# Kernel tuning notes

Measured on AMD Instinct MI355X. Metric: run time of the kernel, lower is better.

The kernel has to match this reference:

```python
import jax, jax.numpy as jnp
import numpy as np

B, T, D, H = 4, 2048, 1024, 16
HD = D // H  # head_dim = 64


def setup_inputs() -> dict:
    key = jax.random.key(0)
    k1, k2, k3, k4, k5 = jax.random.split(key, 5)
    scale = 1.0 / np.sqrt(D)
    return {
        "x": jax.random.normal(k1, (B, T, D), dtype=jnp.float32),
        "mask": jnp.ones((B, T), dtype=jnp.int32),
        "W_qkv": jax.random.normal(k2, (D, 3 * D), dtype=jnp.float32) * scale,
        "b_qkv": jax.random.normal(k3, (3 * D,), dtype=jnp.float32) * 0.01,
        "W_out": jax.random.normal(k4, (D, D), dtype=jnp.float32) * scale,
        "b_out": jax.random.normal(k5, (D,), dtype=jnp.float32) * 0.01,
    }


def reference(x, mask, W_qkv, b_qkv, W_out, b_out):
    Bx, Tx, Dm = x.shape
    qkv = x @ W_qkv + b_qkv                      # [B,T,3D]
    qkv = qkv.reshape(Bx, Tx, 3, H, HD)
    qkv = jnp.transpose(qkv, (2, 0, 3, 1, 4))    # [3,B,H,T,hd]
    q, k, v = qkv[0], qkv[1], qkv[2]
    att = jnp.einsum("bhqd,bhkd->bhqk", q, k) / jnp.sqrt(jnp.float32(HD))
    m = (mask[:, None, None, :] == 0)            # [B,1,1,T]
    att = jnp.where(m, jnp.float32(-1e9), att)
    att = jax.nn.softmax(att, axis=-1)
    out = jnp.einsum("bhqk,bhkd->bhqd", att, v)  # [B,H,T,hd]
    out = jnp.transpose(out, (0, 2, 1, 3)).reshape(Bx, Tx, Dm)
    return out @ W_out + b_out
```

## Files before the change

kernel.cpp:

```cpp
#include <hip/hip_runtime.h>
#include <hip/hip_bf16.h>
#include <stdint.h>

#define B_  4
#define T_  2048
#define D_  1024
#define H_  16
#define HD_ 64

typedef short s16x8 __attribute__((ext_vector_type(8)));
typedef short s16x4 __attribute__((ext_vector_type(4)));
typedef float f32x4 __attribute__((ext_vector_type(4)));

#define MFMA32(a, b, c) __builtin_amdgcn_mfma_f32_16x16x32_bf16(a, b, c, 0, 0, 0)

#if __has_builtin(__builtin_amdgcn_exp2f)
#define FEXP2(x) __builtin_amdgcn_exp2f(x)
#else
#define FEXP2(x) exp2f(x)
#endif

__device__ __forceinline__ unsigned short f2bf(float f) {
    union { float f; unsigned int u; } v; v.f = f;
    unsigned int r = v.u + 0x7fffu + ((v.u >> 16) & 1u);
    return (unsigned short)(r >> 16);
}

__device__ __forceinline__ unsigned int pkbf(float a, float b) {
    __hip_bfloat162 h = __float22bfloat162_rn(float2{a, b});
    union { __hip_bfloat162 h; unsigned int u; } v; v.h = h;
    return v.u;
}

__device__ __forceinline__ void async16(const void* g, void* l) {
    __builtin_amdgcn_global_load_lds(
        (const __attribute__((address_space(1))) unsigned int*)g,
        (__attribute__((address_space(3))) unsigned int*)l, 16, 0, 0);
}

__global__ __launch_bounds__(256)
void prep_kernel(const float* __restrict__ x, unsigned short* __restrict__ xb,
                 const float* __restrict__ Wq, unsigned short* __restrict__ Wqt,
                 const float* __restrict__ Wo, unsigned short* __restrict__ Wot) {
    const int blk = blockIdx.x;
    const int tid = threadIdx.x;
    if (blk < 8192) {
        const int i = blk * 256 + tid;
        float4 v = ((const float4*)x)[i];
        ushort4 o;
        o.x = f2bf(v.x); o.y = f2bf(v.y); o.z = f2bf(v.z); o.w = f2bf(v.w);
        ((ushort4*)xb)[i] = o;
        return;
    }
    __shared__ float t[32][33];
    const float* W; unsigned short* Wt; int K, N, bx, by;
    if (blk < 11264) {
        const int idx = blk - 8192;
        W = Wq; Wt = Wqt; K = 1024; N = 3072;
        bx = (idx % 96) * 32; by = (idx / 96) * 32;
    } else {
        const int idx = blk - 11264;
        W = Wo; Wt = Wot; K = 1024; N = 1024;
        bx = (idx % 32) * 32; by = (idx / 32) * 32;
    }
    const int tx = tid & 31, ty = tid >> 5;
    #pragma unroll
    for (int j = 0; j < 32; j += 8)
        t[ty + j][tx] = W[(size_t)(by + ty + j) * N + bx + tx];
    __syncthreads();
    #pragma unroll
    for (int j = 0; j < 32; j += 8)
        Wt[(size_t)(bx + ty + j) * K + by + tx] = f2bf(t[tx][ty + j]);
}

template <int MODE>
__global__ __launch_bounds__(256)
void gemm_bt_kernel(const unsigned short* __restrict__ A,
                    const unsigned short* __restrict__ Bt,
                    const float* __restrict__ bias,
                    float* __restrict__ Cf,
                    unsigned short* __restrict__ Qo,
                    unsigned short* __restrict__ Ko,
                    unsigned short* __restrict__ Vo,
                    int M, int N, int K) {
    __shared__ __align__(16) unsigned short SMEM[4 * 128 * 64];
    const int tid = threadIdx.x;
    const int w = tid >> 6, lane = tid & 63;
    const int laneN = lane & 15, quad = lane >> 4;
    const int rm0 = blockIdx.x * 128;
    const int rn0 = blockIdx.y * 128;
    const int wr = (w >> 1) * 64, wc = (w & 1) * 64;

    f32x4 acc[4][4] = {};

    auto issueG = [&](int kk, int bufsel) {
        unsigned short* As = SMEM + bufsel * 8192;
        unsigned short* Bs = SMEM + 16384 + bufsel * 8192;
        #pragma unroll
        for (int i = 0; i < 4; ++i) {
            const int c = i * 256 + tid;
            const int row = c >> 3, s = c & 7, g = s ^ (row & 7);
            async16(A + (size_t)(rm0 + row) * K + kk + g * 8,
                    (char*)As + (size_t)c * 16);
        }
        #pragma unroll
        for (int i = 0; i < 4; ++i) {
            const int c = i * 256 + tid;
            const int row = c >> 3, s = c & 7, g = s ^ (row & 7);
            async16(Bt + (size_t)(rn0 + row) * K + kk + g * 8,
                    (char*)Bs + (size_t)c * 16);
        }
    };

    issueG(0, 0);
    const int KI = K >> 6;
    for (int it = 0; it < KI; ++it) {
        const int buf = it & 1;
        __syncthreads();
        const unsigned short* As = SMEM + buf * 8192;
        const unsigned short* Bs = SMEM + 16384 + buf * 8192;
        s16x8 av[2][4], bv[2][4];
        #pragma unroll
        for (int h = 0; h < 2; ++h) {
            #pragma unroll
            for (int ms = 0; ms < 4; ++ms) {
                const int row = wr + ms * 16 + laneN;
                av[h][ms] = *(const s16x8*)&As[row * 64 + ((h * 4 + quad) ^ (row & 7)) * 8];
            }
            #pragma unroll
            for (int ns = 0; ns < 4; ++ns) {
                const int row = wc + ns * 16 + laneN;
                bv[h][ns] = *(const s16x8*)&Bs[row * 64 + ((h * 4 + quad) ^ (row & 7)) * 8];
            }
        }
        if (it + 1 < KI) issueG((it + 1) << 6, buf ^ 1);
        #pragma unroll
        for (int ms = 0; ms < 4; ++ms)
            #pragma unroll
            for (int ns = 0; ns < 4; ++ns) {
                acc[ms][ns] = MFMA32(av[0][ms], bv[0][ns], acc[ms][ns]);
                acc[ms][ns] = MFMA32(av[1][ms], bv[1][ns], acc[ms][ns]);
            }
    }

    if (MODE == 0) {
        #pragma unroll
        for (int ms = 0; ms < 4; ++ms) {
            const int gm0 = rm0 + wr + ms * 16 + quad * 4;
            #pragma unroll
            for (int ns = 0; ns < 4; ++ns) {
                const int gn = rn0 + wc + ns * 16 + laneN;
                const float bb = bias[gn];
                #pragma unroll
                for (int r = 0; r < 4; ++r)
                    Cf[(size_t)(gm0 + r) * N + gn] = acc[ms][ns][r] + bb;
            }
        }
    }
}

__global__ __launch_bounds__(512, 2)
void gemm256x128_qkv_kernel(const unsigned short* __restrict__ A,
                            const unsigned short* __restrict__ Bt,
                            const float* __restrict__ bias,
                            unsigned short* __restrict__ Qo,
                            unsigned short* __restrict__ Ko,
                            unsigned short* __restrict__ Vo,
                            int M, int N, int K) {
    __shared__ __align__(16) unsigned short SMEM[3 * 24576];
    const int tid = threadIdx.x;
    const int w = tid >> 6, lane = tid & 63;
    const int laneN = lane & 15, quad = lane >> 4;
    const int wm = w >> 1, wn = w & 1;
    const int rm0 = blockIdx.x * 256;
    const int rn0 = blockIdx.y * 128;

    f32x4 acc[4][4] = {};

    auto issueTile = [&](int t, int bufsel) {
        const int kk = t << 6;
        unsigned short* As = SMEM + bufsel * 24576;
        unsigned short* Bs = As + 16384;
        #pragma unroll
        for (int i = 0; i < 4; ++i) {
            const int c = i * 512 + tid;
            const int row = c >> 3, s = c & 7, g = s ^ (row & 7);
            async16(A + (size_t)(rm0 + row) * K + kk + g * 8,
                    (char*)As + (size_t)c * 16);
        }
        #pragma unroll
        for (int i = 0; i < 2; ++i) {
            const int c = i * 512 + tid;
            const int row = c >> 3, s = c & 7, g = s ^ (row & 7);
            async16(Bt + (size_t)(rn0 + row) * K + kk + g * 8,
                    (char*)Bs + (size_t)c * 16);
        }
    };

    issueTile(0, 0);
    issueTile(1, 1);
    issueTile(2, 2);
    asm volatile("s_waitcnt vmcnt(12)" ::: "memory");
    __builtin_amdgcn_s_barrier();
    asm volatile("" ::: "memory");

    const int KI = K >> 6;
    int buf = 0;
    for (int kt = 0; kt < KI; ++kt) {
        const unsigned short* As = SMEM + buf * 24576;
        const unsigned short* Bs = As + 16384;
        #pragma unroll
        for (int kh = 0; kh < 2; ++kh) {
            s16x8 av[4], bv[4];
            #pragma unroll
            for (int ns = 0; ns < 4; ++ns) {
                const int row = wn * 64 + ns * 16 + laneN;
                bv[ns] = *(const s16x8*)&Bs[row * 64 + ((kh * 4 + quad) ^ (row & 7)) * 8];
            }
            #pragma unroll
            for (int ms = 0; ms < 4; ++ms) {
                const int row = wm * 64 + ms * 16 + laneN;
                av[ms] = *(const s16x8*)&As[row * 64 + ((kh * 4 + quad) ^ (row & 7)) * 8];
            }
            __builtin_amdgcn_s_setprio(1);
            #pragma unroll
            for (int ms = 0; ms < 4; ++ms)
                #pragma unroll
                for (int ns = 0; ns < 4; ++ns)
                    acc[ms][ns] = MFMA32(av[ms], bv[ns], acc[ms][ns]);
            __builtin_amdgcn_s_setprio(0);
        }
        if (kt + 1 < KI) {
            __builtin_amdgcn_s_barrier();
            asm volatile("" ::: "memory");
            if (kt + 3 < KI) {
                issueTile(kt + 3, buf);
                asm volatile("s_waitcnt vmcnt(12)" ::: "memory");
            } else if (kt + 2 < KI) {
                asm volatile("s_waitcnt vmcnt(6)" ::: "memory");
            } else {
                asm volatile("s_waitcnt vmcnt(0)" ::: "memory");
            }
            __builtin_amdgcn_s_barrier();
            asm volatile("" ::: "memory");
        }
        buf = (buf == 2) ? 0 : buf + 1;
    }

    const int s = rn0 >> 10;
    const int bidx = rm0 >> 11, t0 = rm0 & (T_ - 1);
    if (s < 2) {
        const float fs = (s == 0) ? 0.125f * 1.44269504088896f : 1.0f;
        unsigned short* P = (s == 0) ? Qo : Ko;
        #pragma unroll
        for (int ms = 0; ms < 4; ++ms) {
            const int lm0 = wm * 64 + ms * 16 + quad * 4;
            #pragma unroll
            for (int ns = 0; ns < 4; ++ns) {
                const int gn = rn0 + wn * 64 + ns * 16 + laneN;
                const float bb = bias[gn];
                const int rr = gn & 1023, hh = rr >> 6, dd = rr & 63;
                const size_t base = ((size_t)(bidx * H_ + hh) * T_ + t0);
                #pragma unroll
                for (int r = 0; r < 4; ++r)
                    P[(base + lm0 + r) * HD_ + dd] =
                        f2bf((acc[ms][ns][r] + bb) * fs);
            }
        }
    } else {
        __syncthreads();
        #pragma unroll
        for (int ms = 0; ms < 4; ++ms) {
            const int lm0 = wm * 64 + ms * 16 + quad * 4;
            #pragma unroll
            for (int ns = 0; ns < 4; ++ns) {
                const int nl = wn * 64 + ns * 16 + laneN;
                const float bb = bias[rn0 + nl];
                const int sw = (nl & 7) << 3;
                #pragma unroll
                for (int r = 0; r < 4; ++r)
                    SMEM[nl * 256 + ((lm0 + r) ^ sw)] =
                        f2bf(acc[ms][ns][r] + bb);
            }
        }
        __syncthreads();
        const int nl = tid >> 2, part = tid & 3;
        const int hh = nl >> 6, d = nl & 63;
        const int hAbs = bidx * H_ + ((rn0 & 1023) >> 6) + hh;
        unsigned short* rowp = Vo + ((size_t)hAbs * HD_ + d) * T_ + t0;
        const int swz = nl & 7;
        #pragma unroll
        for (int j = 0; j < 8; ++j) {
            const int mgl = part * 8 + j;
            const int pg = (mgl & 24) | ((mgl & 7) ^ swz);
            const s16x8 vv = *(const s16x8*)&SMEM[nl * 256 + pg * 8];
            *(s16x8*)(rowp + mgl * 8) = vv;
        }
    }
}

__global__ __launch_bounds__(512, 4)
void attn_kernel(const unsigned short* __restrict__ Q,
                 const unsigned short* __restrict__ Kb,
                 const unsigned short* __restrict__ VT,
                 const int* __restrict__ mask,
                 unsigned short* __restrict__ Out) {
    __shared__ __align__(16) unsigned short Ks[2][64 * 64];
    __shared__ __align__(16) unsigned short Vs[2][64 * 64];
    __shared__ float biasF[T_];
    const int tid = threadIdx.x;
    const int lane = tid & 63;
    const int w = tid >> 6;
    const int laneN = lane & 15, quad = lane >> 4;
    const int x7 = laneN & 7;
    const int bh = blockIdx.x;
    const int b = bh >> 4, h = bh & 15;
    const int qbase = blockIdx.y * 256 + w * 32;

    for (int i = tid; i < T_; i += 512)
        biasF[i] = mask[b * T_ + i] ? 0.f : -1.0e9f;

    s16x8 qf[2][2];
    #pragma unroll
    for (int qg = 0; qg < 2; ++qg) {
        const size_t qoff = ((size_t)bh * T_ + qbase + qg * 16 + laneN) * HD_ + quad * 8;
        qf[qg][0] = *(const s16x8*)&Q[qoff];
        qf[qg][1] = *(const s16x8*)&Q[qoff + 32];
    }

    s16x8 ones;
    #pragma unroll
    for (int j = 0; j < 8; ++j) ones[j] = (short)0x3F80;

    const size_t kRow0 = (size_t)bh * T_ * HD_;
    const size_t vRow0 = (size_t)bh * HD_ * T_;

    auto issueTile = [&](int kt, int bufsel) {
        const int kbase = kt * 64;
        {
            const int c = tid;
            const int row = c >> 3, s = c & 7;
            const int fk = (row & 3) | (((row >> 3) & 1) << 2);
            const int g = s ^ fk;
            async16(Kb + kRow0 + (size_t)(kbase + row) * HD_ + g * 8,
                    &Ks[bufsel][c * 8]);
        }
        {
            const int c = tid;
            const int d = c >> 3, s = c & 7, g = s ^ (d & 7);
            async16(VT + vRow0 + (size_t)d * T_ + kbase + g * 8,
                    &Vs[bufsel][c * 8]);
        }
    };

    issueTile(0, 0);

    f32x4 O[2][4] = {};
    f32x4 liacc[2] = {};

    const int rowA = ((laneN >> 2) << 3) + (laneN & 3);

    #pragma unroll 2
    for (int kt = 0; kt < T_ / 64; ++kt) {
        const int buf = kt & 1;
        const int kbase = kt * 64;
        __syncthreads();
        if (kt + 1 < T_ / 64) issueTile(kt + 1, buf ^ 1);

        s16x8 pf[2][2];
        #pragma unroll
        for (int g32 = 0; g32 < 2; ++g32) {
            const int ra = g32 * 32 + rowA;
            const s16x8 kA0 = *(const s16x8*)&Ks[buf][(ra * 8 + (quad ^ x7)) * 8];
            const s16x8 kA1 = *(const s16x8*)&Ks[buf][(ra * 8 + ((4 + quad) ^ x7)) * 8];
            const s16x8 kB0 = *(const s16x8*)&Ks[buf][((ra + 4) * 8 + (quad ^ x7)) * 8];
            const s16x8 kB1 = *(const s16x8*)&Ks[buf][((ra + 4) * 8 + ((4 + quad) ^ x7)) * 8];
            const f32x4 bA = *(const f32x4*)&biasF[kbase + g32 * 32 + quad * 8];
            const f32x4 bB = *(const f32x4*)&biasF[kbase + g32 * 32 + quad * 8 + 4];
            #pragma unroll
            for (int qg = 0; qg < 2; ++qg) {
                f32x4 Sa = bA, Sb = bB;
                Sa = MFMA32(kA0, qf[qg][0], Sa);
                Sa = MFMA32(kA1, qf[qg][1], Sa);
                Sb = MFMA32(kB0, qf[qg][0], Sb);
                Sb = MFMA32(kB1, qf[qg][1], Sb);
                #pragma unroll
                for (int r = 0; r < 4; ++r) {
                    Sa[r] = FEXP2(Sa[r]);
                    Sb[r] = FEXP2(Sb[r]);
                }
                union { s16x8 v; unsigned int u[4]; } pu;
                pu.u[0] = pkbf(Sa[0], Sa[1]);
                pu.u[1] = pkbf(Sa[2], Sa[3]);
                pu.u[2] = pkbf(Sb[0], Sb[1]);
                pu.u[3] = pkbf(Sb[2], Sb[3]);
                pf[qg][g32] = pu.v;
            }
        }

        #pragma unroll
        for (int g32 = 0; g32 < 2; ++g32) {
            s16x8 vf[4];
            #pragma unroll
            for (int nt = 0; nt < 4; ++nt) {
                const int d = nt * 16 + laneN;
                vf[nt] = *(const s16x8*)&Vs[buf][(d * 8 + ((g32 * 4 + quad) ^ x7)) * 8];
            }
            #pragma unroll
            for (int qg = 0; qg < 2; ++qg) {
                #pragma unroll
                for (int nt = 0; nt < 4; ++nt)
                    O[qg][nt] = MFMA32(pf[qg][g32], vf[nt], O[qg][nt]);
                liacc[qg] = MFMA32(pf[qg][g32], ones, liacc[qg]);
            }
        }
    }

    #pragma unroll
    for (int qg = 0; qg < 2; ++qg) {
        #pragma unroll
        for (int r = 0; r < 4; ++r) {
            const float inv = 1.0f / liacc[qg][r];
            const int tq = qbase + qg * 16 + quad * 4 + r;
            #pragma unroll
            for (int nt = 0; nt < 4; ++nt)
                Out[(size_t)(b * T_ + tq) * D_ + h * HD_ + nt * 16 + laneN] =
                    f2bf(O[qg][nt][r] * inv);
        }
    }
}

extern "C" void kernel_launch(void* const* d_in, const int* in_sizes, int n_in,
                              void* d_out, int out_size, void* d_ws, size_t ws_size,
                              hipStream_t stream) {
    const float* x     = (const float*)d_in[0];
    const int*   mask  = (const int*)d_in[1];
    const float* W_qkv = (const float*)d_in[2];
    const float* b_qkv = (const float*)d_in[3];
    const float* W_out = (const float*)d_in[4];
    const float* b_out = (const float*)d_in[5];
    float* out = (float*)d_out;

    unsigned short* ws = (unsigned short*)d_ws;
    const size_t NX = (size_t)B_ * T_ * D_;
    unsigned short* xb  = ws;
    unsigned short* Qb  = xb + NX;
    unsigned short* Kb  = Qb + NX;
    unsigned short* Vtb = Kb + NX;
    unsigned short* Wqt = Vtb + NX;
    unsigned short* Wot = Wqt + (size_t)3 * D_ * D_;
    unsigned short* attn = xb;

    prep_kernel<<<12288, 256, 0, stream>>>(x, xb, W_qkv, Wqt, W_out, Wot);
    gemm256x128_qkv_kernel<<<dim3(B_ * T_ / 256, 3 * D_ / 128), 512, 0, stream>>>(
        xb, Wqt, b_qkv, Qb, Kb, Vtb, B_ * T_, 3 * D_, D_);
    attn_kernel<<<dim3(B_ * H_, T_ / 256), 512, 0, stream>>>(Qb, Kb, Vtb, mask, attn);
    gemm_bt_kernel<0><<<dim3(B_ * T_ / 128, D_ / 128), 256, 0, stream>>>(
        attn, Wot, b_out, out, nullptr, nullptr, nullptr, B_ * T_, D_, D_);
}
```

Before: 266.2 us.

## Restructure QKV GEMM pipeline with per-half barriers and issue-after-compute prefetch

Reworks the triple-buffered QKV GEMM main loop. The wait and barrier now come at the top of each iteration, and the next tile is issued after both k-halves finish computing. Barriers are added around each MFMA cluster so all waves run their MFMA phases in lockstep, a ping-pong style schedule meant to overlap LDS reads and matrix math across waves. This adds more barriers per iteration and delays when the prefetch is issued.

Result: no change. 263.8 us (-0.9%).

```diff
diff --git a/kernel.cpp b/kernel.cpp
--- a/kernel.cpp
+++ b/kernel.cpp
@@ -160,13 +160,13 @@
 }
 
 __global__ __launch_bounds__(512, 2)
-void gemm256x128_qkv_kernel(const unsigned short* __restrict__ A,
-                            const unsigned short* __restrict__ Bt,
-                            const float* __restrict__ bias,
-                            unsigned short* __restrict__ Qo,
-                            unsigned short* __restrict__ Ko,
-                            unsigned short* __restrict__ Vo,
-                            int M, int N, int K) {
+void gemm_fp_qkv_kernel(const unsigned short* __restrict__ A,
+                        const unsigned short* __restrict__ Bt,
+                        const float* __restrict__ bias,
+                        unsigned short* __restrict__ Qo,
+                        unsigned short* __restrict__ Ko,
+                        unsigned short* __restrict__ Vo,
+                        int M, int N, int K) {
     __shared__ __align__(16) unsigned short SMEM[3 * 24576];
     const int tid = threadIdx.x;
     const int w = tid >> 6, lane = tid & 63;
@@ -177,9 +177,9 @@
 
     f32x4 acc[4][4] = {};
 
-    auto issueTile = [&](int t, int bufsel) {
+    auto issueTile = [&](int t) {
         const int kk = t << 6;
-        unsigned short* As = SMEM + bufsel * 24576;
+        unsigned short* As = SMEM + (t % 3) * 24576;
         unsigned short* Bs = As + 16384;
         #pragma unroll
         for (int i = 0; i < 4; ++i) {
@@ -197,18 +197,19 @@
         }
     };
 
-    issueTile(0, 0);
-    issueTile(1, 1);
-    issueTile(2, 2);
-    asm volatile("s_waitcnt vmcnt(12)" ::: "memory");
-    __builtin_amdgcn_s_barrier();
-    asm volatile("" ::: "memory");
+    issueTile(0);
+    issueTile(1);
+    issueTile(2);
 
     const int KI = K >> 6;
-    int buf = 0;
-    for (int kt = 0; kt < KI; ++kt) {
-        const unsigned short* As = SMEM + buf * 24576;
+    for (int u = 0; u < KI; ++u) {
+        const unsigned short* As = SMEM + (u % 3) * 24576;
         const unsigned short* Bs = As + 16384;
+        if (u < KI - 2)      asm volatile("s_waitcnt vmcnt(12)" ::: "memory");
+        else if (u == KI - 2) asm volatile("s_waitcnt vmcnt(6)" ::: "memory");
+        else                  asm volatile("s_waitcnt vmcnt(0)" ::: "memory");
+        __builtin_amdgcn_s_barrier();
+        asm volatile("" ::: "memory");
         #pragma unroll
         for (int kh = 0; kh < 2; ++kh) {
             s16x8 av[4], bv[4];
@@ -222,6 +223,9 @@
                 const int row = wm * 64 + ms * 16 + laneN;
                 av[ms] = *(const s16x8*)&As[row * 64 + ((kh * 4 + quad) ^ (row & 7)) * 8];
             }
+            asm volatile("" ::: "memory");
+            __builtin_amdgcn_s_barrier();
+            asm volatile("" ::: "memory");
             __builtin_amdgcn_s_setprio(1);
             #pragma unroll
             for (int ms = 0; ms < 4; ++ms)
@@ -229,22 +233,10 @@
                 for (int ns = 0; ns < 4; ++ns)
                     acc[ms][ns] = MFMA32(av[ms], bv[ns], acc[ms][ns]);
             __builtin_amdgcn_s_setprio(0);
-        }
-        if (kt + 1 < KI) {
             __builtin_amdgcn_s_barrier();
             asm volatile("" ::: "memory");
-            if (kt + 3 < KI) {
-                issueTile(kt + 3, buf);
-                asm volatile("s_waitcnt vmcnt(12)" ::: "memory");
-            } else if (kt + 2 < KI) {
-                asm volatile("s_waitcnt vmcnt(6)" ::: "memory");
-            } else {
-                asm volatile("s_waitcnt vmcnt(0)" ::: "memory");
-            }
-            __builtin_amdgcn_s_barrier();
-            asm volatile("" ::: "memory");
-        }
-        buf = (buf == 2) ? 0 : buf + 1;
+        }
+        if (u + 3 < KI) issueTile(u + 3);
     }
 
     const int s = rn0 >> 10;
@@ -452,7 +444,7 @@
     unsigned short* attn = xb;
 
     prep_kernel<<<12288, 256, 0, stream>>>(x, xb, W_qkv, Wqt, W_out, Wot);
-    gemm256x128_qkv_kernel<<<dim3(B_ * T_ / 256, 3 * D_ / 128), 512, 0, stream>>>(
+    gemm_fp_qkv_kernel<<<dim3(B_ * T_ / 256, 3 * D_ / 128), 512, 0, stream>>>(
         xb, Wqt, b_qkv, Qb, Kb, Vtb, B_ * T_, 3 * D_, D_);
     attn_kernel<<<dim3(B_ * H_, T_ / 256), 512, 0, stream>>>(Qb, Kb, Vtb, mask, attn);
     gemm_bt_kernel<0><<<dim3(B_ * T_ / 128, D_ / 128), 256, 0, stream>>>(
```
